# Optimization experiments

Hardware: AMD Instinct MI355X
Metric: run time of the kernel (lower is better)

The kernel has to match this reference:

```python
import jax, jax.numpy as jnp
import numpy as np

EMBED_DIM = 1024
NUM_HEADS = 16
HEAD_DIM = EMBED_DIM // NUM_HEADS
B, N = 4, 2048


def setup_inputs() -> dict:
    key = jax.random.key(0)
    k = jax.random.split(key, 5)
    scale = 1.0 / np.sqrt(EMBED_DIM)
    return {
        "x": jax.random.normal(k[0], (B, N, EMBED_DIM), dtype=jnp.float32),
        # torch nn.Linear convention: y = x @ W.T + b, W shape [out, in]
        "qkv_w": jax.random.uniform(k[1], (3 * EMBED_DIM, EMBED_DIM), jnp.float32, -scale, scale),
        "qkv_b": jax.random.uniform(k[2], (3 * EMBED_DIM,), jnp.float32, -scale, scale),
        "out_w": jax.random.uniform(k[3], (EMBED_DIM, EMBED_DIM), jnp.float32, -scale, scale),
        "out_b": jax.random.uniform(k[4], (EMBED_DIM,), jnp.float32, -scale, scale),
    }


def reference(x, qkv_w, qkv_b, out_w, out_b):
    b, n, e = x.shape
    qkv = x @ qkv_w.T + qkv_b                      # [B,N,3E]
    qkv = qkv.reshape(b, n, 3, NUM_HEADS, HEAD_DIM)
    qkv = jnp.transpose(qkv, (2, 0, 3, 1, 4))      # [3,B,H,N,D]
    q, k, v = qkv[0], qkv[1], qkv[2]
    scores = jnp.einsum("bhqd,bhkd->bhqk", q, k) / np.sqrt(HEAD_DIM)
    weights = jax.nn.softmax(scores, axis=-1)
    attn = jnp.einsum("bhqk,bhkd->bhqd", weights, v)  # [B,H,N,D]
    attn = jnp.transpose(attn, (0, 2, 1, 3)).reshape(b, n, e)
    return attn @ out_w.T + out_b
```

## Files before the change

### kernel.cpp

```cpp
#include <hip/hip_runtime.h>
#include <hip/hip_bf16.h>

#define EMBED 1024
#define NHEADS 16
#define HDIM 64
#define BATCH 4
#define SEQ 2048
#define MROWS (BATCH*SEQ)
#define QKVN (3*EMBED)
#define KDIM 1024

typedef __bf16 bf16;
typedef __bf16 bf16x4 __attribute__((ext_vector_type(4)));
typedef __bf16 bf16x8 __attribute__((ext_vector_type(8)));
typedef float f32x4 __attribute__((ext_vector_type(4)));
typedef float f32x16 __attribute__((ext_vector_type(16)));

#define QSCALE 0.18033688011112042f

#define NX (MROWS*EMBED/4)
#define NQ (QKVN*KDIM/4)
#define NO (EMBED*KDIM/4)
__global__ void cvt_all(const float* __restrict__ x, const float* __restrict__ qw,
                        const float* __restrict__ ow,
                        bf16* __restrict__ xb, bf16* __restrict__ qwb, bf16* __restrict__ owb) {
    int i = blockIdx.x * blockDim.x + threadIdx.x;
    const float* src; bf16* dst; int j;
    if (i < NX)            { src = x;  dst = xb;  j = i; }
    else if (i < NX + NQ)  { src = qw; dst = qwb; j = i - NX; }
    else if (i < NX+NQ+NO) { src = ow; dst = owb; j = i - NX - NQ; }
    else return;
    float4 f = ((const float4*)src)[j];
    bf16x4 o;
    o[0] = (bf16)f.x; o[1] = (bf16)f.y; o[2] = (bf16)f.z; o[3] = (bf16)f.w;
    *((bf16x4*)dst + j) = o;
}

template<int MODE>
__launch_bounds__(256)
__global__ void gemm_bt(const bf16* __restrict__ A, const bf16* __restrict__ B,
                        const float* __restrict__ bias,
                        float* __restrict__ outF,
                        bf16* __restrict__ Qb, bf16* __restrict__ Kb, bf16* __restrict__ Vt)
{
    __shared__ __align__(16) char ldsmem[16384];
    bf16 (*Alds)[32] = (bf16(*)[32])ldsmem;
    bf16 (*Blds)[32] = (bf16(*)[32])(ldsmem + 8192);
    bf16* bounce = (bf16*)ldsmem;

    const int tid = threadIdx.x;
    const int l = tid & 63, w = tid >> 6;
    const int wr = w >> 1, wc = w & 1;
    const int tM = blockIdx.y * 128, tN = blockIdx.x * 128;

    f32x4 acc[4][4] = {};
    const bf16* Abase = A + (size_t)tM * KDIM;
    const bf16* Bbase = B + (size_t)tN * KDIM;

    for (int k0 = 0; k0 < KDIM; k0 += 32) {
        #pragma unroll
        for (int t = 0; t < 2; ++t) {
            int idx = t * 256 + tid;
            int row = idx >> 2;
            int kc = (idx & 3) * 8;
            __builtin_amdgcn_global_load_lds(
                (const __attribute__((address_space(1))) void*)(Abase + (size_t)row * KDIM + k0 + kc),
                (__attribute__((address_space(3))) void*)((char*)&Alds[0][0] + idx * 16),
                16, 0, 0);
            __builtin_amdgcn_global_load_lds(
                (const __attribute__((address_space(1))) void*)(Bbase + (size_t)row * KDIM + k0 + kc),
                (__attribute__((address_space(3))) void*)((char*)&Blds[0][0] + idx * 16),
                16, 0, 0);
        }
        __syncthreads();
        bf16x8 a[4], b[4];
        #pragma unroll
        for (int i = 0; i < 4; ++i)
            a[i] = *(const bf16x8*)&Alds[wr * 64 + i * 16 + (l & 15)][(l >> 4) * 8];
        #pragma unroll
        for (int j = 0; j < 4; ++j)
            b[j] = *(const bf16x8*)&Blds[wc * 64 + j * 16 + (l & 15)][(l >> 4) * 8];
        #pragma unroll
        for (int i = 0; i < 4; ++i)
            #pragma unroll
            for (int j = 0; j < 4; ++j)
                acc[i][j] = __builtin_amdgcn_mfma_f32_16x16x32_bf16(a[i], b[j], acc[i][j], 0, 0, 0);
        __syncthreads();
    }

    if (MODE == 1) {
        #pragma unroll
        for (int i = 0; i < 4; ++i) {
            #pragma unroll
            for (int j = 0; j < 4; ++j) {
                int n = tN + wc * 64 + j * 16 + (l & 15);
                float bv = bias[n];
                #pragma unroll
                for (int r = 0; r < 4; ++r) {
                    int m = tM + wr * 64 + i * 16 + (l >> 4) * 4 + r;
                    outF[(size_t)m * EMBED + n] = acc[i][j][r] + bv;
                }
            }
        }
    } else {
        const int which = tN >> 10;
        const int bidx  = tM >> 11;
        const int hd0   = (tN & 1023) >> 6;
        const int t32base = (tM & 2047) >> 5;
        bf16* dstbase = (which == 0) ? Qb : (which == 1) ? Kb : Vt;
        const float scale = (which == 0) ? QSCALE : 1.0f;

        float bj[4];
        #pragma unroll
        for (int j = 0; j < 4; ++j)
            bj[j] = bias[tN + wc * 64 + j * 16 + (l & 15)];

        #pragma unroll
        for (int pass = 0; pass < 2; ++pass) {
            __syncthreads();
            #pragma unroll
            for (int ii = 0; ii < 2; ++ii) {
                const int i = pass * 2 + ii;
                #pragma unroll
                for (int j = 0; j < 4; ++j) {
                    const int d = (wc * 64 + j * 16 + (l & 15)) & 63;
                    #pragma unroll
                    for (int r = 0; r < 4; ++r) {
                        const int nsl = wr * 64 + i * 16 + (l >> 4) * 4 + r;
                        float v = acc[i][j][r] + bj[j];
                        int off;
                        if (which == 2) {
                            int dblk = d >> 5;
                            int rem16 = nsl & 15;
                            int c = (nsl >> 4) & 1;
                            int fj = (rem16 & 3) | ((rem16 & 8) >> 1);
                            int fhi = (rem16 >> 2) & 1;
                            int lane = (d & 31) | (fhi << 5);
                            off = (dblk * 2 + c) * 512 + lane * 8 + fj;
                        } else {
                            int kk = d >> 4, fhi = (d >> 3) & 1, fj = d & 7;
                            int lane = (nsl & 31) | (fhi << 5);
                            off = kk * 512 + lane * 8 + fj;
                        }
                        bounce[(wc * 2 + wr) * 2048 + off] = (bf16)(v * scale);
                    }
                }
            }
            __syncthreads();
            const int chunk = tid >> 6;
            size_t gbase = ((size_t)(bidx * NHEADS + hd0 + (chunk >> 1)) * 64
                            + t32base + 2 * (chunk & 1) + pass) * 2048;
            #pragma unroll
            for (int s = 0; s < 4; ++s) {
                int eoff = s * 512 + (tid & 63) * 8;
                *(bf16x8*)(dstbase + gbase + eoff) = *(const bf16x8*)&bounce[chunk * 2048 + eoff];
            }
        }
    }
}

__launch_bounds__(256)
__global__ void gemm_bt64(const bf16* __restrict__ A, const bf16* __restrict__ B,
                          const float* __restrict__ bias, float* __restrict__ outF)
{
    __shared__ bf16 Alds[64][32];
    __shared__ bf16 Blds[128][32];
    const int tid = threadIdx.x;
    const int l = tid & 63, w = tid >> 6;
    const int tM = blockIdx.y * 64, tN = blockIdx.x * 128;

    f32x4 acc[4][2] = {};
    const bf16* Abase = A + (size_t)tM * KDIM;
    const bf16* Bbase = B + (size_t)tN * KDIM;

    for (int k0 = 0; k0 < KDIM; k0 += 32) {
        {
            int row = tid >> 2;
            int kc = (tid & 3) * 8;
            __builtin_amdgcn_global_load_lds(
                (const __attribute__((address_space(1))) void*)(Abase + (size_t)row * KDIM + k0 + kc),
                (__attribute__((address_space(3))) void*)((char*)&Alds[0][0] + tid * 16),
                16, 0, 0);
        }
        #pragma unroll
        for (int t = 0; t < 2; ++t) {
            int idx = t * 256 + tid;
            int row = idx >> 2;
            int kc = (idx & 3) * 8;
            __builtin_amdgcn_global_load_lds(
                (const __attribute__((address_space(1))) void*)(Bbase + (size_t)row * KDIM + k0 + kc),
                (__attribute__((address_space(3))) void*)((char*)&Blds[0][0] + idx * 16),
                16, 0, 0);
        }
        __syncthreads();
        bf16x8 a[4], b[2];
        #pragma unroll
        for (int i = 0; i < 4; ++i)
            a[i] = *(const bf16x8*)&Alds[i * 16 + (l & 15)][(l >> 4) * 8];
        #pragma unroll
        for (int j = 0; j < 2; ++j)
            b[j] = *(const bf16x8*)&Blds[w * 32 + j * 16 + (l & 15)][(l >> 4) * 8];
        #pragma unroll
        for (int i = 0; i < 4; ++i)
            #pragma unroll
            for (int j = 0; j < 2; ++j)
                acc[i][j] = __builtin_amdgcn_mfma_f32_16x16x32_bf16(a[i], b[j], acc[i][j], 0, 0, 0);
        __syncthreads();
    }

    #pragma unroll
    for (int i = 0; i < 4; ++i) {
        #pragma unroll
        for (int j = 0; j < 2; ++j) {
            int n = tN + w * 32 + j * 16 + (l & 15);
            float bv = bias[n];
            #pragma unroll
            for (int r = 0; r < 4; ++r) {
                int m = tM + i * 16 + (l >> 4) * 4 + r;
                outF[(size_t)m * EMBED + n] = acc[i][j][r] + bv;
            }
        }
    }
}

static __device__ __forceinline__ unsigned cvt_pk(float lo, float hi) {
    unsigned r;
    asm("v_cvt_pk_bf16_f32 %0, %1, %2" : "=v"(r) : "v"(lo), "v"(hi));
    return r;
}

__launch_bounds__(256, 4)
__global__ void attn_kernel(const bf16* __restrict__ Qb, const bf16* __restrict__ Kb,
                            const bf16* __restrict__ Vt, bf16* __restrict__ AO)
{
    __shared__ bf16 kv[2][2][2048];
    const int tid = threadIdx.x, l = tid & 63, w = tid >> 6;
    const int lo5 = l & 31, hi = l >> 5;
    int bid = blockIdx.x;
    int swz = (bid & 7) * 128 + (bid >> 3);
    const int bh = swz >> 4;
    const int qt = swz & 15;

    const bf16* QFh = Qb + (size_t)bh * (64 * 2048);
    const bf16* Ksrc = Kb + (size_t)bh * (64 * 2048) + w * 512 + l * 8;
    const bf16* Vsrc = Vt + (size_t)bh * (64 * 2048) + w * 512 + l * 8;

    const int qtile = qt * 4 + w;
    const bf16* qbase = QFh + (size_t)qtile * 2048 + (size_t)l * 8;
    bf16x8 qf[4];
    #pragma unroll
    for (int kk = 0; kk < 4; ++kk)
        qf[kk] = *(const bf16x8*)(qbase + kk * 512);

    f32x16 O0 = {}, O1 = {};
    float lsum = 0.f;

#define STAGE(BUF)                                                                       \
    {                                                                                    \
        __builtin_amdgcn_global_load_lds(                                                \
            (const __attribute__((address_space(1))) void*)Ksrc,                         \
            (__attribute__((address_space(3))) void*)&kv[BUF][0][w * 512], 16, 0, 0);    \
        __builtin_amdgcn_global_load_lds(                                                \
            (const __attribute__((address_space(1))) void*)Vsrc,                         \
            (__attribute__((address_space(3))) void*)&kv[BUF][1][w * 512], 16, 0, 0);    \
        Ksrc += 2048; Vsrc += 2048;                                                      \
    }

    STAGE(0)
    __syncthreads();

#define ATTN_BODY(B)                                                                     \
    {                                                                                    \
        STAGE(B ^ 1)                                                                     \
        bf16x8 kK0 = *(const bf16x8*)&kv[B][0][0 * 512 + l * 8];                         \
        bf16x8 kK1 = *(const bf16x8*)&kv[B][0][1 * 512 + l * 8];                         \
        bf16x8 kK2 = *(const bf16x8*)&kv[B][0][2 * 512 + l * 8];                         \
        bf16x8 kK3 = *(const bf16x8*)&kv[B][0][3 * 512 + l * 8];                         \
        bf16x8 vf00 = *(const bf16x8*)&kv[B][1][0 * 512 + l * 8];                        \
        bf16x8 vf01 = *(const bf16x8*)&kv[B][1][1 * 512 + l * 8];                        \
        bf16x8 vf10 = *(const bf16x8*)&kv[B][1][2 * 512 + l * 8];                        \
        bf16x8 vf11 = *(const bf16x8*)&kv[B][1][3 * 512 + l * 8];                        \
        f32x16 S = {};                                                                   \
        __builtin_amdgcn_s_setprio(1);                                                   \
        S = __builtin_amdgcn_mfma_f32_32x32x16_bf16(kK0, qf[0], S, 0, 0, 0);             \
        S = __builtin_amdgcn_mfma_f32_32x32x16_bf16(kK1, qf[1], S, 0, 0, 0);             \
        S = __builtin_amdgcn_mfma_f32_32x32x16_bf16(kK2, qf[2], S, 0, 0, 0);             \
        S = __builtin_amdgcn_mfma_f32_32x32x16_bf16(kK3, qf[3], S, 0, 0, 0);             \
        __builtin_amdgcn_s_setprio(0);                                                   \
        float p[16];                                                                     \
        _Pragma("unroll")                                                                \
        for (int r = 0; r < 16; ++r)                                                     \
            p[r] = __builtin_amdgcn_exp2f(S[r]);                                         \
        float s0 = (p[0] + p[1]) + (p[2] + p[3]);                                        \
        float s1 = (p[4] + p[5]) + (p[6] + p[7]);                                        \
        float s2 = (p[8] + p[9]) + (p[10] + p[11]);                                      \
        float s3 = (p[12] + p[13]) + (p[14] + p[15]);                                    \
        lsum += (s0 + s1) + (s2 + s3);                                                   \
        union { unsigned u[4]; bf16x8 v; } pk0, pk1;                                     \
        pk0.u[0] = cvt_pk(p[0], p[1]);   pk0.u[1] = cvt_pk(p[2], p[3]);                  \
        pk0.u[2] = cvt_pk(p[4], p[5]);   pk0.u[3] = cvt_pk(p[6], p[7]);                  \
        pk1.u[0] = cvt_pk(p[8], p[9]);   pk1.u[1] = cvt_pk(p[10], p[11]);                \
        pk1.u[2] = cvt_pk(p[12], p[13]); pk1.u[3] = cvt_pk(p[14], p[15]);                \
        __builtin_amdgcn_s_setprio(1);                                                   \
        O0 = __builtin_amdgcn_mfma_f32_32x32x16_bf16(vf00, pk0.v, O0, 0, 0, 0);          \
        O0 = __builtin_amdgcn_mfma_f32_32x32x16_bf16(vf01, pk1.v, O0, 0, 0, 0);          \
        O1 = __builtin_amdgcn_mfma_f32_32x32x16_bf16(vf10, pk0.v, O1, 0, 0, 0);          \
        O1 = __builtin_amdgcn_mfma_f32_32x32x16_bf16(vf11, pk1.v, O1, 0, 0, 0);          \
        __builtin_amdgcn_s_setprio(0);                                                   \
        __syncthreads();                                                                 \
    }

    for (int t2 = 0; t2 < 64; t2 += 2) {
        ATTN_BODY(0)
        ATTN_BODY(1)
    }
#undef ATTN_BODY
#undef STAGE

    lsum += __shfl_xor(lsum, 32);
    float linv = 1.0f / lsum;

    const int b = bh >> 4, hd = bh & 15;
    const int q0 = qt * 128 + w * 32;
    bf16* outp = &AO[(size_t)(b * SEQ + q0 + lo5) * EMBED + hd * HDIM];
    #pragma unroll
    for (int g = 0; g < 4; ++g) {
        bf16x4 o0, o1;
        #pragma unroll
        for (int r4 = 0; r4 < 4; ++r4) {
            o0[r4] = (bf16)(O0[g * 4 + r4] * linv);
            o1[r4] = (bf16)(O1[g * 4 + r4] * linv);
        }
        *(bf16x4*)&outp[g * 8 + hi * 4] = o0;
        *(bf16x4*)&outp[32 + g * 8 + hi * 4] = o1;
    }
}

extern "C" void kernel_launch(void* const* d_in, const int* in_sizes, int n_in,
                              void* d_out, int out_size, void* d_ws, size_t ws_size,
                              hipStream_t stream) {
    const float* x     = (const float*)d_in[0];
    const float* qkv_w = (const float*)d_in[1];
    const float* qkv_b = (const float*)d_in[2];
    const float* out_w = (const float*)d_in[3];
    const float* out_b = (const float*)d_in[4];
    float* out = (float*)d_out;

    char* ws = (char*)d_ws;
    bf16* xb  = (bf16*)(ws);
    bf16* qwb = (bf16*)(ws + 16777216);
    bf16* owb = (bf16*)(ws + 23068672);
    bf16* Qb  = (bf16*)(ws + 25165824);
    bf16* Kb  = (bf16*)(ws + 41943040);
    bf16* Vt  = (bf16*)(ws + 58720256);
    bf16* AO  = (bf16*)(ws + 75497472);

    cvt_all<<<(NX + NQ + NO + 255) / 256, 256, 0, stream>>>(x, qkv_w, out_w, xb, qwb, owb);

    gemm_bt<0><<<dim3(QKVN / 128, MROWS / 128), 256, 0, stream>>>(
        xb, qwb, qkv_b, nullptr, Qb, Kb, Vt);

    attn_kernel<<<BATCH * NHEADS * (SEQ / 128), 256, 0, stream>>>(Qb, Kb, Vt, AO);

    gemm_bt64<<<dim3(EMBED / 128, MROWS / 64), 256, 0, stream>>>(AO, owb, out_b, out);
}
```

Baseline: 191.7 us.

## Double-buffer GEMM LDS stages and swizzle QKV epilogue bounce buffer

Both GEMM kernels now use two LDS buffers, issuing async global-to-LDS loads for the next K slice while MFMAs run on the current one. Synchronization uses explicit waitcnt and s_barrier calls with sched barriers. The QKV epilogue bounce buffer gets an XOR swizzle to cut LDS bank conflicts. This doubles LDS per block, which may lower occupancy, and it relies on hand-set vmcnt counts being correct.

```diff
diff --git a/kernel.cpp b/kernel.cpp
--- a/kernel.cpp
+++ b/kernel.cpp
@@ -17,6 +17,8 @@
 typedef float f32x16 __attribute__((ext_vector_type(16)));
 
 #define QSCALE 0.18033688011112042f
+
+#define SWB(B) ((B) ^ ((((B) >> 9) & 1) << 4) ^ ((((B) >> 7) & 1) << 5))
 
 #define NX (MROWS*EMBED/4)
 #define NQ (QKVN*KDIM/4)
@@ -36,17 +38,17 @@
     *((bf16x4*)dst + j) = o;
 }
 
-template<int MODE>
 __launch_bounds__(256)
-__global__ void gemm_bt(const bf16* __restrict__ A, const bf16* __restrict__ B,
-                        const float* __restrict__ bias,
-                        float* __restrict__ outF,
-                        bf16* __restrict__ Qb, bf16* __restrict__ Kb, bf16* __restrict__ Vt)
+__global__ void gemm_qkv(const bf16* __restrict__ A, const bf16* __restrict__ B,
+                         const float* __restrict__ bias,
+                         bf16* __restrict__ Qb, bf16* __restrict__ Kb, bf16* __restrict__ Vt)
 {
-    __shared__ __align__(16) char ldsmem[16384];
-    bf16 (*Alds)[32] = (bf16(*)[32])ldsmem;
-    bf16 (*Blds)[32] = (bf16(*)[32])(ldsmem + 8192);
-    bf16* bounce = (bf16*)ldsmem;
+    __shared__ __align__(16) char ldsmem[32768];
+    char* A0 = ldsmem;
+    char* B0 = ldsmem + 8192;
+    char* A1 = ldsmem + 16384;
+    char* B1 = ldsmem + 24576;
+    char* bnc = ldsmem;
 
     const int tid = threadIdx.x;
     const int l = tid & 63, w = tid >> 6;
@@ -57,114 +59,128 @@
     const bf16* Abase = A + (size_t)tM * KDIM;
     const bf16* Bbase = B + (size_t)tN * KDIM;
 
-    for (int k0 = 0; k0 < KDIM; k0 += 32) {
+#define GSTAGE(AL, BL, KOFF)                                                             \
+    {                                                                                    \
+        int koff_ = (KOFF) < KDIM ? (KOFF) : 0;                                          \
+        _Pragma("unroll")                                                                \
+        for (int t = 0; t < 2; ++t) {                                                    \
+            int idx = t * 256 + tid;                                                     \
+            int row = idx >> 2;                                                          \
+            int kc = (idx & 3) * 8;                                                      \
+            __builtin_amdgcn_global_load_lds(                                            \
+                (const __attribute__((address_space(1))) void*)(Abase + (size_t)row * KDIM + koff_ + kc), \
+                (__attribute__((address_space(3))) void*)((AL) + idx * 16), 16, 0, 0);   \
+            __builtin_amdgcn_global_load_lds(                                            \
+                (const __attribute__((address_space(1))) void*)(Bbase + (size_t)row * KDIM + koff_ + kc), \
+                (__attribute__((address_space(3))) void*)((BL) + idx * 16), 16, 0, 0);   \
+        }                                                                                \
+    }
+
+#define GBODY(AL, BL, KNEXT)                                                             \
+    {                                                                                    \
+        bf16x8 a[4], b[4];                                                               \
+        _Pragma("unroll")                                                                \
+        for (int i = 0; i < 4; ++i)                                                      \
+            a[i] = *(const bf16x8*)((AL) + ((wr * 64 + i * 16 + (l & 15)) * 32 + (l >> 4) * 8) * 2); \
+        _Pragma("unroll")                                                                \
+        for (int j = 0; j < 4; ++j)                                                      \
+            b[j] = *(const bf16x8*)((BL) + ((wc * 64 + j * 16 + (l & 15)) * 32 + (l >> 4) * 8) * 2); \
+        asm volatile("s_waitcnt lgkmcnt(0)" ::: "memory");                               \
+        __builtin_amdgcn_sched_barrier(0);                                               \
+        __builtin_amdgcn_s_barrier();                                                    \
+        __builtin_amdgcn_sched_barrier(0);                                               \
+        GSTAGE(AL, BL, KNEXT)                                                            \
+        _Pragma("unroll")                                                                \
+        for (int i = 0; i < 4; ++i)                                                      \
+            _Pragma("unroll")                                                            \
+            for (int j = 0; j < 4; ++j)                                                  \
+                acc[i][j] = __builtin_amdgcn_mfma_f32_16x16x32_bf16(a[i], b[j], acc[i][j], 0, 0, 0); \
+        asm volatile("s_waitcnt vmcnt(4)" ::: "memory");                                 \
+        __builtin_amdgcn_sched_barrier(0);                                               \
+        __builtin_amdgcn_s_barrier();                                                    \
+        __builtin_amdgcn_sched_barrier(0);                                               \
+    }
+
+    GSTAGE(A0, B0, 0)
+    GSTAGE(A1, B1, 32)
+    asm volatile("s_waitcnt vmcnt(4)" ::: "memory");
+    __builtin_amdgcn_sched_barrier(0);
+    __builtin_amdgcn_s_barrier();
+    __builtin_amdgcn_sched_barrier(0);
+
+    for (int k0 = 0; k0 < KDIM; k0 += 64) {
+        GBODY(A0, B0, k0 + 64)
+        GBODY(A1, B1, k0 + 96)
+    }
+#undef GBODY
+#undef GSTAGE
+
+    const int which = tN >> 10;
+    const int bidx  = tM >> 11;
+    const int hd0   = (tN & 1023) >> 6;
+    const int t32base = (tM & 2047) >> 5;
+    bf16* dstbase = (which == 0) ? Qb : (which == 1) ? Kb : Vt;
+    const float scale = (which == 0) ? QSCALE : 1.0f;
+
+    float bj[4];
+    #pragma unroll
+    for (int j = 0; j < 4; ++j)
+        bj[j] = bias[tN + wc * 64 + j * 16 + (l & 15)];
+
+    #pragma unroll
+    for (int pass = 0; pass < 2; ++pass) {
+        __syncthreads();
         #pragma unroll
-        for (int t = 0; t < 2; ++t) {
-            int idx = t * 256 + tid;
-            int row = idx >> 2;
-            int kc = (idx & 3) * 8;
-            __builtin_amdgcn_global_load_lds(
-                (const __attribute__((address_space(1))) void*)(Abase + (size_t)row * KDIM + k0 + kc),
-                (__attribute__((address_space(3))) void*)((char*)&Alds[0][0] + idx * 16),
-                16, 0, 0);
-            __builtin_amdgcn_global_load_lds(
-                (const __attribute__((address_space(1))) void*)(Bbase + (size_t)row * KDIM + k0 + kc),
-                (__attribute__((address_space(3))) void*)((char*)&Blds[0][0] + idx * 16),
-                16, 0, 0);
-        }
-        __syncthreads();
-        bf16x8 a[4], b[4];
-        #pragma unroll
-        for (int i = 0; i < 4; ++i)
-            a[i] = *(const bf16x8*)&Alds[wr * 64 + i * 16 + (l & 15)][(l >> 4) * 8];
-        #pragma unroll
-        for (int j = 0; j < 4; ++j)
-            b[j] = *(const bf16x8*)&Blds[wc * 64 + j * 16 + (l & 15)][(l >> 4) * 8];
-        #pragma unroll
-        for (int i = 0; i < 4; ++i)
-            #pragma unroll
-            for (int j = 0; j < 4; ++j)
-                acc[i][j] = __builtin_amdgcn_mfma_f32_16x16x32_bf16(a[i], b[j], acc[i][j], 0, 0, 0);
-        __syncthreads();
-    }
-
-    if (MODE == 1) {
-        #pragma unroll
-        for (int i = 0; i < 4; ++i) {
+        for (int ii = 0; ii < 2; ++ii) {
+            const int i = pass * 2 + ii;
             #pragma unroll
             for (int j = 0; j < 4; ++j) {
-                int n = tN + wc * 64 + j * 16 + (l & 15);
-                float bv = bias[n];
+                const int d = (wc * 64 + j * 16 + (l & 15)) & 63;
                 #pragma unroll
                 for (int r = 0; r < 4; ++r) {
-                    int m = tM + wr * 64 + i * 16 + (l >> 4) * 4 + r;
-                    outF[(size_t)m * EMBED + n] = acc[i][j][r] + bv;
+                    const int nsl = wr * 64 + i * 16 + (l >> 4) * 4 + r;
+                    float v = acc[i][j][r] + bj[j];
+                    int off;
+                    if (which == 2) {
+                        int dblk = d >> 5;
+                        int rem16 = nsl & 15;
+                        int c = (nsl >> 4) & 1;
+                        int fj = (rem16 & 3) | ((rem16 & 8) >> 1);
+                        int fhi = (rem16 >> 2) & 1;
+                        int lane = (d & 31) | (fhi << 5);
+                        off = (dblk * 2 + c) * 512 + lane * 8 + fj;
+                    } else {
+                        int kk = d >> 4, fhi = (d >> 3) & 1, fj = d & 7;
+                        int lane = (nsl & 31) | (fhi << 5);
+                        off = kk * 512 + lane * 8 + fj;
+                    }
+                    *(bf16*)(bnc + (wc * 2 + wr) * 4096 + SWB(off * 2)) = (bf16)(v * scale);
                 }
             }
         }
-    } else {
-        const int which = tN >> 10;
-        const int bidx  = tM >> 11;
-        const int hd0   = (tN & 1023) >> 6;
-        const int t32base = (tM & 2047) >> 5;
-        bf16* dstbase = (which == 0) ? Qb : (which == 1) ? Kb : Vt;
-        const float scale = (which == 0) ? QSCALE : 1.0f;
-
-        float bj[4];
+        __syncthreads();
+        const int chunk = tid >> 6;
+        size_t gbase = ((size_t)(bidx * NHEADS + hd0 + (chunk >> 1)) * 64
+                        + t32base + 2 * (chunk & 1) + pass) * 2048;
         #pragma unroll
-        for (int j = 0; j < 4; ++j)
-            bj[j] = bias[tN + wc * 64 + j * 16 + (l & 15)];
-
-        #pragma unroll
-        for (int pass = 0; pass < 2; ++pass) {
-            __syncthreads();
-            #pragma unroll
-            for (int ii = 0; ii < 2; ++ii) {
-                const int i = pass * 2 + ii;
-                #pragma unroll
-                for (int j = 0; j < 4; ++j) {
-                    const int d = (wc * 64 + j * 16 + (l & 15)) & 63;
-                    #pragma unroll
-                    for (int r = 0; r < 4; ++r) {
-                        const int nsl = wr * 64 + i * 16 + (l >> 4) * 4 + r;
-                        float v = acc[i][j][r] + bj[j];
-                        int off;
-                        if (which == 2) {
-                            int dblk = d >> 5;
-                            int rem16 = nsl & 15;
-                            int c = (nsl >> 4) & 1;
-                            int fj = (rem16 & 3) | ((rem16 & 8) >> 1);
-                            int fhi = (rem16 >> 2) & 1;
-                            int lane = (d & 31) | (fhi << 5);
-                            off = (dblk * 2 + c) * 512 + lane * 8 + fj;
-                        } else {
-                            int kk = d >> 4, fhi = (d >> 3) & 1, fj = d & 7;
-                            int lane = (nsl & 31) | (fhi << 5);
-                            off = kk * 512 + lane * 8 + fj;
-                        }
-                        bounce[(wc * 2 + wr) * 2048 + off] = (bf16)(v * scale);
-                    }
-                }
-            }
-            __syncthreads();
-            const int chunk = tid >> 6;
-            size_t gbase = ((size_t)(bidx * NHEADS + hd0 + (chunk >> 1)) * 64
-                            + t32base + 2 * (chunk & 1) + pass) * 2048;
-            #pragma unroll
-            for (int s = 0; s < 4; ++s) {
-                int eoff = s * 512 + (tid & 63) * 8;
-                *(bf16x8*)(dstbase + gbase + eoff) = *(const bf16x8*)&bounce[chunk * 2048 + eoff];
-            }
+        for (int s = 0; s < 4; ++s) {
+            int boff = SWB((s * 512 + (tid & 63) * 8) * 2);
+            *(bf16x8*)(dstbase + gbase + s * 0 + 0 + ((size_t)0)) ;
+            *(bf16x8*)(dstbase + gbase + (size_t)(s * 512 + (tid & 63) * 8)) =
+                *(const bf16x8*)(bnc + chunk * 4096 + boff);
         }
     }
 }
 
 __launch_bounds__(256)
-__global__ void gemm_bt64(const bf16* __restrict__ A, const bf16* __restrict__ B,
-                          const float* __restrict__ bias, float* __restrict__ outF)
+__global__ void gemm_out(const bf16* __restrict__ A, const bf16* __restrict__ B,
+                         const float* __restrict__ bias, float* __restrict__ outF)
 {
-    __shared__ bf16 Alds[64][32];
-    __shared__ bf16 Blds[128][32];
+    __shared__ __align__(16) char lds64[24576];
+    char* A0 = lds64;
+    char* B0 = lds64 + 4096;
+    char* A1 = lds64 + 12288;
+    char* B1 = lds64 + 16384;
     const int tid = threadIdx.x;
     const int l = tid & 63, w = tid >> 6;
     const int tM = blockIdx.y * 64, tN = blockIdx.x * 128;
@@ -173,40 +189,65 @@
     const bf16* Abase = A + (size_t)tM * KDIM;
     const bf16* Bbase = B + (size_t)tN * KDIM;
 
-    for (int k0 = 0; k0 < KDIM; k0 += 32) {
-        {
-            int row = tid >> 2;
-            int kc = (tid & 3) * 8;
-            __builtin_amdgcn_global_load_lds(
-                (const __attribute__((address_space(1))) void*)(Abase + (size_t)row * KDIM + k0 + kc),
-                (__attribute__((address_space(3))) void*)((char*)&Alds[0][0] + tid * 16),
-                16, 0, 0);
-        }
-        #pragma unroll
-        for (int t = 0; t < 2; ++t) {
-            int idx = t * 256 + tid;
-            int row = idx >> 2;
-            int kc = (idx & 3) * 8;
-            __builtin_amdgcn_global_load_lds(
-                (const __attribute__((address_space(1))) void*)(Bbase + (size_t)row * KDIM + k0 + kc),
-                (__attribute__((address_space(3))) void*)((char*)&Blds[0][0] + idx * 16),
-                16, 0, 0);
-        }
-        __syncthreads();
-        bf16x8 a[4], b[2];
-        #pragma unroll
-        for (int i = 0; i < 4; ++i)
-            a[i] = *(const bf16x8*)&Alds[i * 16 + (l & 15)][(l >> 4) * 8];
-        #pragma unroll
-        for (int j = 0; j < 2; ++j)
-            b[j] = *(const bf16x8*)&Blds[w * 32 + j * 16 + (l & 15)][(l >> 4) * 8];
-        #pragma unroll
-        for (int i = 0; i < 4; ++i)
-            #pragma unroll
-            for (int j = 0; j < 2; ++j)
-                acc[i][j] = __builtin_amdgcn_mfma_f32_16x16x32_bf16(a[i], b[j], acc[i][j], 0, 0, 0);
-        __syncthreads();
-    }
+#define OSTAGE(AL, BL, KOFF)                                                             \
+    {                                                                                    \
+        int koff_ = (KOFF) < KDIM ? (KOFF) : 0;                                          \
+        {                                                                                \
+            int row = tid >> 2;                                                          \
+            int kc = (tid & 3) * 8;                                                      \
+            __builtin_amdgcn_global_load_lds(                                            \
+                (const __attribute__((address_space(1))) void*)(Abase + (size_t)row * KDIM + koff_ + kc), \
+                (__attribute__((address_space(3))) void*)((AL) + tid * 16), 16, 0, 0);   \
+        }                                                                                \
+        _Pragma("unroll")                                                                \
+        for (int t = 0; t < 2; ++t) {                                                    \
+            int idx = t * 256 + tid;                                                     \
+            int row = idx >> 2;                                                          \
+            int kc = (idx & 3) * 8;                                                      \
+            __builtin_amdgcn_global_load_lds(                                            \
+                (const __attribute__((address_space(1))) void*)(Bbase + (size_t)row * KDIM + koff_ + kc), \
+                (__attribute__((address_space(3))) void*)((BL) + idx * 16), 16, 0, 0);   \
+        }                                                                                \
+    }
+
+#define OBODY(AL, BL, KNEXT)                                                             \
+    {                                                                                    \
+        bf16x8 a[4], b[2];                                                               \
+        _Pragma("unroll")                                                                \
+        for (int i = 0; i < 4; ++i)                                                      \
+            a[i] = *(const bf16x8*)((AL) + ((i * 16 + (l & 15)) * 32 + (l >> 4) * 8) * 2); \
+        _Pragma("unroll")                                                                \
+        for (int j = 0; j < 2; ++j)                                                      \
+            b[j] = *(const bf16x8*)((BL) + ((w * 32 + j * 16 + (l & 15)) * 32 + (l >> 4) * 8) * 2); \
+        asm volatile("s_waitcnt lgkmcnt(0)" ::: "memory");                               \
+        __builtin_amdgcn_sched_barrier(0);                                               \
+        __builtin_amdgcn_s_barrier();                                                    \
+        __builtin_amdgcn_sched_barrier(0);                                               \
+        OSTAGE(AL, BL, KNEXT)                                                            \
+        _Pragma("unroll")                                                                \
+        for (int i = 0; i < 4; ++i)                                                      \
+            _Pragma("unroll")                                                            \
+            for (int j = 0; j < 2; ++j)                                                  \
+                acc[i][j] = __builtin_amdgcn_mfma_f32_16x16x32_bf16(a[i], b[j], acc[i][j], 0, 0, 0); \
+        asm volatile("s_waitcnt vmcnt(3)" ::: "memory");                                 \
+        __builtin_amdgcn_sched_barrier(0);                                               \
+        __builtin_amdgcn_s_barrier();                                                    \
+        __builtin_amdgcn_sched_barrier(0);                                               \
+    }
+
+    OSTAGE(A0, B0, 0)
+    OSTAGE(A1, B1, 32)
+    asm volatile("s_waitcnt vmcnt(3)" ::: "memory");
+    __builtin_amdgcn_sched_barrier(0);
+    __builtin_amdgcn_s_barrier();
+    __builtin_amdgcn_sched_barrier(0);
+
+    for (int k0 = 0; k0 < KDIM; k0 += 64) {
+        OBODY(A0, B0, k0 + 64)
+        OBODY(A1, B1, k0 + 96)
+    }
+#undef OBODY
+#undef OSTAGE
 
     #pragma unroll
     for (int i = 0; i < 4; ++i) {
@@ -357,10 +398,10 @@
 
     cvt_all<<<(NX + NQ + NO + 255) / 256, 256, 0, stream>>>(x, qkv_w, out_w, xb, qwb, owb);
 
-    gemm_bt<0><<<dim3(QKVN / 128, MROWS / 128), 256, 0, stream>>>(
-        xb, qwb, qkv_b, nullptr, Qb, Kb, Vt);
+    gemm_qkv<<<dim3(QKVN / 128, MROWS / 128), 256, 0, stream>>>(
+        xb, qwb, qkv_b, Qb, Kb, Vt);
 
     attn_kernel<<<BATCH * NHEADS * (SEQ / 128), 256, 0, stream>>>(Qb, Kb, Vt, AO);
 
-    gemm_bt64<<<dim3(EMBED / 128, MROWS / 64), 256, 0, stream>>>(AO, owb, out_b, out);
-}
+    gemm_out<<<dim3(EMBED / 128, MROWS / 64), 256, 0, stream>>>(AO, owb, out_b, out);
+}
```

Result: faster. 186.8 us (-2.5%).
